# Kernel optimization log

Measured on AMD Instinct MI355X. Metric: run time of the kernel, lower is better.

The kernel has to match this reference:

```python
import jax, jax.numpy as jnp
import numpy as np

A, NL, LD, F, W, DEPTH = 128, 16, 256, 256, 1024, 4
CH, CHD = 8, 64   # cross-attn heads / head_dim
SH, SHD = 8, 32   # latent self-attn heads / head_dim
FF = 256          # 2**ceil(log2(latent_dim))
FLAT = NL * LD


def _ln(x, g, b, eps=1e-5):
    m = x.mean(-1, keepdims=True)
    v = ((x - m) ** 2).mean(-1, keepdims=True)
    return (x - m) * jax.lax.rsqrt(v + eps) * g + b


def _attn(q_in, kv, wq, wk, wv, wo, bo, h, hd):
    b, s, _ = q_in.shape
    t = kv.shape[1]
    q = (q_in @ wq.T).reshape(b, s, h, hd)
    k = (kv @ wk.T).reshape(b, t, h, hd)
    v = (kv @ wv.T).reshape(b, t, h, hd)
    p = jax.nn.softmax(jnp.einsum('bihd,bjhd->bhij', q, k) * (hd ** -0.5), axis=-1)
    o = jnp.einsum('bhij,bjhd->bihd', p, v).reshape(b, s, h * hd)
    return o @ wo.T + bo


def _block(q, kv, p, h, hd):
    wq, wk, wv, wo, bo, g1, b1, fw1, fb1, fw2, fb2, g2, b2 = p
    z = _ln(q + _attn(q, kv, wq, wk, wv, wo, bo, h, hd), g1, b1)
    ff = jax.nn.relu(z @ fw1.T + fb1) @ fw2.T + fb2
    return _ln(z + ff, g2, b2)


def setup_inputs() -> dict:
    key = jax.random.key(0)
    ks = iter(jax.random.split(key, 40))
    def rn(shape, s=0.02):
        return jax.random.normal(next(ks), shape, jnp.float32) * s
    return {
        'x': jax.random.normal(next(ks), (A, W, F), jnp.float32),
        'z': jax.random.normal(next(ks), (A, NL, LD), jnp.float32),
        'c_wq': rn((CH * CHD, LD)), 'c_wk': rn((CH * CHD, F)), 'c_wv': rn((CH * CHD, F)),
        'c_wo': rn((LD, CH * CHD)), 'c_bo': jnp.zeros((LD,), jnp.float32),
        'c_ln1_g': jnp.ones((LD,), jnp.float32), 'c_ln1_b': jnp.zeros((LD,), jnp.float32),
        'c_ff_w1': rn((FF, LD)), 'c_ff_b1': jnp.zeros((FF,), jnp.float32),
        'c_ff_w2': rn((LD, FF)), 'c_ff_b2': jnp.zeros((LD,), jnp.float32),
        'c_ln2_g': jnp.ones((LD,), jnp.float32), 'c_ln2_b': jnp.zeros((LD,), jnp.float32),
        's_wq': rn((DEPTH, SH * SHD, LD)), 's_wk': rn((DEPTH, SH * SHD, LD)),
        's_wv': rn((DEPTH, SH * SHD, LD)), 's_wo': rn((DEPTH, LD, SH * SHD)),
        's_bo': jnp.zeros((DEPTH, LD), jnp.float32),
        's_ln1_g': jnp.ones((DEPTH, LD), jnp.float32), 's_ln1_b': jnp.zeros((DEPTH, LD), jnp.float32),
        's_ff_w1': rn((DEPTH, FF, LD)), 's_ff_b1': jnp.zeros((DEPTH, FF), jnp.float32),
        's_ff_w2': rn((DEPTH, LD, FF)), 's_ff_b2': jnp.zeros((DEPTH, LD), jnp.float32),
        's_ln2_g': jnp.ones((DEPTH, LD), jnp.float32), 's_ln2_b': jnp.zeros((DEPTH, LD), jnp.float32),
        'q_w': rn((FLAT, FLAT)), 'q_b': jnp.zeros((FLAT,), jnp.float32),
        'k_w': rn((FLAT, FLAT)), 'k_b': jnp.zeros((FLAT,), jnp.float32),
        'v_w': rn((FLAT, FLAT)), 'v_b': jnp.zeros((FLAT,), jnp.float32),
    }


def reference(x, z, c_wq, c_wk, c_wv, c_wo, c_bo, c_ln1_g, c_ln1_b, c_ff_w1, c_ff_b1,
              c_ff_w2, c_ff_b2, c_ln2_g, c_ln2_b,
              s_wq, s_wk, s_wv, s_wo, s_bo, s_ln1_g, s_ln1_b, s_ff_w1, s_ff_b1,
              s_ff_w2, s_ff_b2, s_ln2_g, s_ln2_b,
              q_w, q_b, k_w, k_b, v_w, v_b):
    z_prior = z
    # NOTE: original LSRE.forward computes cross-attention but assigns the
    # result to x and never uses it. Replicated faithfully (dead computation;
    # output does not depend on x or the cross-attn params).
    _ = _block(z, x, (c_wq, c_wk, c_wv, c_wo, c_bo, c_ln1_g, c_ln1_b,
                      c_ff_w1, c_ff_b1, c_ff_w2, c_ff_b2, c_ln2_g, c_ln2_b), CH, CHD)
    zc = z
    sp = (s_wq, s_wk, s_wv, s_wo, s_bo, s_ln1_g, s_ln1_b,
          s_ff_w1, s_ff_b1, s_ff_w2, s_ff_b2, s_ln2_g, s_ln2_b)
    for i in range(DEPTH):
        zc = _block(zc, zc, tuple(p[i] for p in sp), SH, SHD)
    # CANN: asset-to-asset attention; broadcast-mul-then-sum == attn @ v
    zf = zc.reshape(A, FLAT)
    q = zf @ q_w.T + q_b
    k = zf @ k_w.T + k_b
    v = zf @ v_w.T + v_b
    attn = jax.nn.softmax((q @ k.T) * (LD ** -0.5), axis=-1)
    h = (attn @ v).reshape(A, NL, LD)
    return (h, z_prior)
```

## Files before the change

kernel.cpp:

```cpp
#include <hip/hip_runtime.h>
#include <math.h>

typedef __bf16 bf16x8 __attribute__((ext_vector_type(8)));
typedef __bf16 bf16x4 __attribute__((ext_vector_type(4)));
typedef float  f32x4  __attribute__((ext_vector_type(4)));

#define MFMA(a,b,c) __builtin_amdgcn_mfma_f32_16x16x32_bf16((a),(b),(c),0,0,0)

#define A_N   128
#define LDIM  256
#define FLATD 4096

__global__ void k_cvt_w(const float* __restrict__ s0, const float* __restrict__ s1,
                        const float* __restrict__ s2, const float* __restrict__ s3,
                        const float* __restrict__ s4, const float* __restrict__ s5,
                        __bf16* __restrict__ dh, __bf16* __restrict__ dl) {
    const float* s;
    switch (blockIdx.y) {
        case 0: s = s0; break; case 1: s = s1; break; case 2: s = s2; break;
        case 3: s = s3; break; case 4: s = s4; break; default: s = s5; break;
    }
    size_t off  = (size_t)blockIdx.x * 2048 + threadIdx.x * 8;
    const float4* sp = (const float4*)(s + off);
    float4 x = sp[0], y = sp[1];
    float v[8] = {x.x, x.y, x.z, x.w, y.x, y.y, y.z, y.w};
    bf16x8 h, l;
    #pragma unroll
    for (int j = 0; j < 8; ++j) {
        __bf16 hh = (__bf16)v[j];
        h[j] = hh;
        l[j] = (__bf16)(v[j] - (float)hh);
    }
    size_t dst = (size_t)blockIdx.y * 262144 + off;
    *(bf16x8*)(dh + dst) = h;
    *(bf16x8*)(dl + dst) = l;
}

__global__ __launch_bounds__(1024) void k_latent(
    const float* __restrict__ z,
    const __bf16* __restrict__ Wh, const __bf16* __restrict__ Wl,
    const float* __restrict__ boa,
    const float* __restrict__ g1a, const float* __restrict__ b1a,
    const float* __restrict__ fb1a, const float* __restrict__ fb2a,
    const float* __restrict__ g2a, const float* __restrict__ b2a,
    float* __restrict__ zprior, __bf16* __restrict__ Zbh, __bf16* __restrict__ Zbl)
{
    __shared__ __align__(16) char arena[57856];
    float*  zf  = (float*)arena;
    __bf16* zbh = (__bf16*)(arena + 16384);
    __bf16* zbl = (__bf16*)(arena + 24832);
    __bf16* Ph  = (__bf16*)(arena + 16384);
    __bf16* Qh  = (__bf16*)(arena + 33280);
    __bf16* ob  = Qh;
    __bf16* Kh  = (__bf16*)(arena + 41472);
    __bf16* Vt  = (__bf16*)(arena + 49664);

    const int a    = blockIdx.x;
    const int t    = threadIdx.x;
    const int w    = t >> 6;
    const int lane = t & 63;
    const int q    = lane >> 4;
    const int r    = lane & 15;
    const int nc   = w * 16;
    const int head = w >> 1;
    const int hc   = (w & 1) * 16;

    {
        int row = t >> 6, col = (t & 63) * 4;
        const float4 x = *(const float4*)(z + (size_t)a * 4096 + row * 256 + col);
        *(float4*)(zprior + (size_t)a * 4096 + row * 256 + col) = x;
        float v[4] = {x.x, x.y, x.z, x.w};
        float*  zr = zf  + row * 256 + col;
        __bf16* zh = zbh + row * 264 + col;
        __bf16* zl = zbl + row * 264 + col;
        #pragma unroll
        for (int j = 0; j < 4; ++j) {
            zr[j] = v[j];
            __bf16 hh = (__bf16)v[j];
            zh[j] = hh;
            zl[j] = (__bf16)(v[j] - (float)hh);
        }
    }
    __syncthreads();

    auto do_ln = [&](const float* g, const float* bb) {
        int col = lane * 4;
        float* zr = zf + w * 256 + col;
        float4 v4 = *(const float4*)zr;
        float v[4] = {v4.x, v4.y, v4.z, v4.w};
        float s1 = 0.f, s2 = 0.f;
        #pragma unroll
        for (int j = 0; j < 4; ++j) { s1 += v[j]; s2 += v[j]*v[j]; }
        #pragma unroll
        for (int o = 1; o <= 32; o <<= 1) {
            s1 += __shfl_xor(s1, o);
            s2 += __shfl_xor(s2, o);
        }
        float mean = s1 * (1.0f/256.0f);
        float var  = s2 * (1.0f/256.0f) - mean * mean;
        float inv  = rsqrtf(var + 1e-5f);
        float4 g4 = *(const float4*)(g + col);
        float4 b4 = *(const float4*)(bb + col);
        float gg[4] = {g4.x, g4.y, g4.z, g4.w};
        float bbv[4] = {b4.x, b4.y, b4.z, b4.w};
        __bf16* zh = zbh + w * 264 + col;
        __bf16* zl = zbl + w * 264 + col;
        float y[4];
        #pragma unroll
        for (int j = 0; j < 4; ++j) {
            y[j] = (v[j] - mean) * inv * gg[j] + bbv[j];
            __bf16 hh = (__bf16)y[j];
            zh[j] = hh;
            zl[j] = (__bf16)(y[j] - (float)hh);
        }
        *(float4*)zr = (float4){y[0], y[1], y[2], y[3]};
    };

    const f32x4 zero4 = {0.f, 0.f, 0.f, 0.f};
    bf16x8 zer8;
    #pragma unroll
    for (int j = 0; j < 8; ++j) zer8[j] = (__bf16)0.0f;

    for (int lp = 0; lp < 4; ++lp) {
        const size_t lo0 = (size_t)lp * 65536;
        const __bf16* wqh = Wh + 0*262144 + lo0; const __bf16* wql = Wl + 0*262144 + lo0;
        const __bf16* wkh = Wh + 1*262144 + lo0; const __bf16* wkl = Wl + 1*262144 + lo0;
        const __bf16* wvh = Wh + 2*262144 + lo0; const __bf16* wvl = Wl + 2*262144 + lo0;
        const __bf16* woh = Wh + 3*262144 + lo0; const __bf16* wol = Wl + 3*262144 + lo0;
        const __bf16* f1h = Wh + 4*262144 + lo0; const __bf16* f1l = Wl + 4*262144 + lo0;
        const __bf16* f2h = Wh + 5*262144 + lo0; const __bf16* f2l = Wl + 5*262144 + lo0;
        const float* bo  = boa  + lp*256;
        const float* g1  = g1a  + lp*256; const float* b1 = b1a + lp*256;
        const float* fb1 = fb1a + lp*256; const float* fb2 = fb2a + lp*256;
        const float* g2  = g2a  + lp*256; const float* b2 = b2a + lp*256;

        const size_t wrow = (size_t)(nc + r) * 256 + q * 8;
        const __bf16* zA_h = zbh + r * 264 + q * 8;
        const __bf16* zA_l = zbl + r * 264 + q * 8;
        const __bf16* oA   = ob  + r * 264 + q * 8;

        {
            const __bf16* pq_h = wqh + wrow; const __bf16* pq_l = wql + wrow;
            const __bf16* pk_h = wkh + wrow; const __bf16* pk_l = wkl + wrow;
            const __bf16* pv_h = wvh + wrow; const __bf16* pv_l = wvl + wrow;
            f32x4 aq = zero4, ak = zero4, av = zero4;
            #pragma unroll
            for (int ks = 0; ks < 8; ++ks) {
                bf16x8 afh = *(const bf16x8*)(zA_h + ks*32);
                bf16x8 afl = *(const bf16x8*)(zA_l + ks*32);
                bf16x8 qh = *(const bf16x8*)(pq_h + ks*32);
                bf16x8 ql = *(const bf16x8*)(pq_l + ks*32);
                bf16x8 kh = *(const bf16x8*)(pk_h + ks*32);
                bf16x8 kl = *(const bf16x8*)(pk_l + ks*32);
                bf16x8 vh = *(const bf16x8*)(pv_h + ks*32);
                bf16x8 vl = *(const bf16x8*)(pv_l + ks*32);
                aq = MFMA(afh, qh, aq); aq = MFMA(afl, qh, aq); aq = MFMA(afh, ql, aq);
                ak = MFMA(afh, kh, ak); ak = MFMA(afl, kh, ak); ak = MFMA(afh, kl, ak);
                av = MFMA(afh, vh, av); av = MFMA(afl, vh, av); av = MFMA(afh, vl, av);
            }
            #pragma unroll
            for (int i = 0; i < 4; ++i) {
                int m = q*4 + i;
                Qh[(head*16 + m)*32 + hc + r] = (__bf16)aq[i];
                Kh[(head*16 + m)*32 + hc + r] = (__bf16)ak[i];
                Vt[(head*32 + hc + r)*16 + m] = (__bf16)av[i];
            }
        }
        __syncthreads();

        if (w < 8) {
            bf16x8 qa = *(const bf16x8*)(Qh + (w*16 + r)*32 + q*8);
            bf16x8 ka = *(const bf16x8*)(Kh + (w*16 + r)*32 + q*8);
            f32x4 s = MFMA(qa, ka, zero4);
            #pragma unroll
            for (int i = 0; i < 4; ++i) {
                float sc = s[i] * 0.17677669529663687f;
                float mx = sc;
                #pragma unroll
                for (int o = 1; o <= 8; o <<= 1) mx = fmaxf(mx, __shfl_xor(mx, o, 16));
                float e = __expf(sc - mx);
                float sm = e;
                #pragma unroll
                for (int o = 1; o <= 8; o <<= 1) sm += __shfl_xor(sm, o, 16);
                Ph[(w*16 + q*4 + i)*32 + r]      = (__bf16)(e / sm);
                Ph[(w*16 + q*4 + i)*32 + 16 + r] = (__bf16)0.0f;
            }
        }
        __syncthreads();

        {
            int ph = w & 7, vnt = w >> 3;
            bf16x8 pa = *(const bf16x8*)(Ph + (ph*16 + r)*32 + q*8);
            bf16x8 vb = (q < 2)
                ? *(const bf16x8*)(Vt + (ph*32 + vnt*16 + r)*16 + q*8) : zer8;
            f32x4 o = MFMA(pa, vb, zero4);
            #pragma unroll
            for (int i = 0; i < 4; ++i)
                ob[(q*4 + i)*264 + ph*32 + vnt*16 + r] = (__bf16)o[i];
        }
        __syncthreads();

        {
            const __bf16* po_h = woh + wrow; const __bf16* po_l = wol + wrow;
            f32x4 acc = zero4;
            #pragma unroll
            for (int ks = 0; ks < 8; ++ks) {
                bf16x8 af = *(const bf16x8*)(oA + ks*32);
                bf16x8 bh = *(const bf16x8*)(po_h + ks*32);
                bf16x8 bl = *(const bf16x8*)(po_l + ks*32);
                acc = MFMA(af, bh, acc);
                acc = MFMA(af, bl, acc);
            }
            #pragma unroll
            for (int i = 0; i < 4; ++i) {
                int row = q*4 + i, col = nc + r;
                zf[row*256 + col] = acc[i] + bo[col] + zf[row*256 + col];
            }
        }
        __syncthreads();
        do_ln(g1, b1);
        __syncthreads();

        {
            const __bf16* pf_h = f1h + wrow; const __bf16* pf_l = f1l + wrow;
            f32x4 acc = zero4;
            #pragma unroll
            for (int ks = 0; ks < 8; ++ks) {
                bf16x8 afh = *(const bf16x8*)(zA_h + ks*32);
                bf16x8 afl = *(const bf16x8*)(zA_l + ks*32);
                bf16x8 bh  = *(const bf16x8*)(pf_h + ks*32);
                bf16x8 bl  = *(const bf16x8*)(pf_l + ks*32);
                acc = MFMA(afh, bh, acc);
                acc = MFMA(afl, bh, acc);
                acc = MFMA(afh, bl, acc);
            }
            #pragma unroll
            for (int i = 0; i < 4; ++i) {
                int row = q*4 + i, col = nc + r;
                ob[row*264 + col] = (__bf16)fmaxf(acc[i] + fb1[col], 0.0f);
            }
        }
        __syncthreads();

        {
            const __bf16* pf_h = f2h + wrow; const __bf16* pf_l = f2l + wrow;
            f32x4 acc = zero4;
            #pragma unroll
            for (int ks = 0; ks < 8; ++ks) {
                bf16x8 af = *(const bf16x8*)(oA + ks*32);
                bf16x8 bh = *(const bf16x8*)(pf_h + ks*32);
                bf16x8 bl = *(const bf16x8*)(pf_l + ks*32);
                acc = MFMA(af, bh, acc);
                acc = MFMA(af, bl, acc);
            }
            #pragma unroll
            for (int i = 0; i < 4; ++i) {
                int row = q*4 + i, col = nc + r;
                zf[row*256 + col] = acc[i] + fb2[col] + zf[row*256 + col];
            }
        }
        __syncthreads();
        do_ln(g2, b2);
        __syncthreads();
    }

    {
        int row = t >> 6, col = (t & 63) * 4;
        *(bf16x4*)(Zbh + (size_t)a * 4096 + row * 256 + col) =
            *(const bf16x4*)(zbh + row * 264 + col);
        *(bf16x4*)(Zbl + (size_t)a * 4096 + row * 256 + col) =
            *(const bf16x4*)(zbl + row * 264 + col);
    }
}

__global__ __launch_bounds__(256) void k_cann_gemm(
    const __bf16* __restrict__ Zh, const __bf16* __restrict__ Zl,
    const float* __restrict__ W0, const float* __restrict__ W1, const float* __restrict__ W2,
    const float* __restrict__ b0, const float* __restrict__ b1, const float* __restrict__ b2,
    float* __restrict__ C0, float* __restrict__ C1, float* __restrict__ C2)
{
    const float* W; const float* bias; float* C;
    if (blockIdx.y == 0)      { W = W0; bias = b0; C = C0; }
    else if (blockIdx.y == 1) { W = W1; bias = b1; C = C1; }
    else                      { W = W2; bias = b2; C = C2; }

    __shared__ __bf16 Ash[128 * 72];
    __shared__ __bf16 Asl[128 * 72];
    __shared__ __bf16 Bsh[32 * 72];
    __shared__ __bf16 Bsl[32 * 72];

    const int t = threadIdx.x;
    const int w = t >> 6, lane = t & 63, q = lane >> 4, r = lane & 15;
    const int n0 = blockIdx.x * 32;
    const int m0 = w * 32;
    const int br = t >> 3, bc = t & 7;

    const f32x4 zero4 = {0.f, 0.f, 0.f, 0.f};
    f32x4 acc[2][2] = {{zero4, zero4}, {zero4, zero4}};

    for (int k0 = 0; k0 < FLATD; k0 += 64) {
        #pragma unroll
        for (int l = 0; l < 4; ++l) {
            int idx = t + l * 256;
            int rr = idx >> 3, cc = idx & 7;
            *(bf16x8*)(Ash + rr*72 + cc*8) =
                *(const bf16x8*)(Zh + (size_t)rr * FLATD + k0 + cc*8);
            *(bf16x8*)(Asl + rr*72 + cc*8) =
                *(const bf16x8*)(Zl + (size_t)rr * FLATD + k0 + cc*8);
        }
        {
            const float4* wp = (const float4*)(W + (size_t)(n0 + br) * FLATD + k0 + bc*8);
            float4 x = wp[0], y = wp[1];
            float v[8] = {x.x, x.y, x.z, x.w, y.x, y.y, y.z, y.w};
            bf16x8 h, l;
            #pragma unroll
            for (int j = 0; j < 8; ++j) {
                __bf16 hh = (__bf16)v[j];
                h[j] = hh;
                l[j] = (__bf16)(v[j] - (float)hh);
            }
            *(bf16x8*)(Bsh + br*72 + bc*8) = h;
            *(bf16x8*)(Bsl + br*72 + bc*8) = l;
        }
        __syncthreads();
        #pragma unroll
        for (int ks = 0; ks < 2; ++ks) {
            bf16x8 a0h = *(const bf16x8*)(Ash + (m0 + r)*72      + ks*32 + q*8);
            bf16x8 a1h = *(const bf16x8*)(Ash + (m0 + 16 + r)*72 + ks*32 + q*8);
            bf16x8 a0l = *(const bf16x8*)(Asl + (m0 + r)*72      + ks*32 + q*8);
            bf16x8 a1l = *(const bf16x8*)(Asl + (m0 + 16 + r)*72 + ks*32 + q*8);
            bf16x8 g0h = *(const bf16x8*)(Bsh + r*72             + ks*32 + q*8);
            bf16x8 g1h = *(const bf16x8*)(Bsh + (16 + r)*72      + ks*32 + q*8);
            bf16x8 g0l = *(const bf16x8*)(Bsl + r*72             + ks*32 + q*8);
            bf16x8 g1l = *(const bf16x8*)(Bsl + (16 + r)*72      + ks*32 + q*8);
            acc[0][0] = MFMA(a0h, g0h, acc[0][0]);
            acc[0][0] = MFMA(a0l, g0h, acc[0][0]);
            acc[0][0] = MFMA(a0h, g0l, acc[0][0]);
            acc[0][1] = MFMA(a0h, g1h, acc[0][1]);
            acc[0][1] = MFMA(a0l, g1h, acc[0][1]);
            acc[0][1] = MFMA(a0h, g1l, acc[0][1]);
            acc[1][0] = MFMA(a1h, g0h, acc[1][0]);
            acc[1][0] = MFMA(a1l, g0h, acc[1][0]);
            acc[1][0] = MFMA(a1h, g0l, acc[1][0]);
            acc[1][1] = MFMA(a1h, g1h, acc[1][1]);
            acc[1][1] = MFMA(a1l, g1h, acc[1][1]);
            acc[1][1] = MFMA(a1h, g1l, acc[1][1]);
        }
        __syncthreads();
    }

    if (blockIdx.y == 1) {
        #pragma unroll
        for (int mi = 0; mi < 2; ++mi)
            #pragma unroll
            for (int ni = 0; ni < 2; ++ni)
                #pragma unroll
                for (int i = 0; i < 4; ++i) {
                    int row = m0 + mi*16 + q*4 + i;
                    int col = n0 + ni*16 + r;
                    C[(size_t)col * 128 + row] = acc[mi][ni][i] + bias[col];
                }
    } else {
        #pragma unroll
        for (int mi = 0; mi < 2; ++mi)
            #pragma unroll
            for (int ni = 0; ni < 2; ++ni)
                #pragma unroll
                for (int i = 0; i < 4; ++i) {
                    int row = m0 + mi*16 + q*4 + i;
                    int col = n0 + ni*16 + r;
                    C[(size_t)row * FLATD + col] = acc[mi][ni][i] + bias[col];
                }
    }
}

__global__ __launch_bounds__(512) void k_cann_scores(const float* __restrict__ Q,
                              const float* __restrict__ KT,
                              float* __restrict__ P) {
    const int i = blockIdx.x;
    const int t = threadIdx.x;
    __shared__ float qrow[FLATD];
    __shared__ float part[4][128];
    __shared__ float wred[2];
    __shared__ float wsum[2];
    {
        const float4* src = (const float4*)(Q + (size_t)i * FLATD);
        float4* dst = (float4*)qrow;
        dst[t]       = src[t];
        dst[t + 512] = src[t + 512];
    }
    __syncthreads();

    const int j = t & 127, quarter = t >> 7;
    const float* kp = KT + (size_t)quarter * 1024 * 128 + j;
    const float* qp = qrow + quarter * 1024;
    float sc = 0.0f;
    #pragma unroll 8
    for (int k = 0; k < 1024; ++k) sc += qp[k] * kp[(size_t)k * 128];
    part[quarter][j] = sc;
    __syncthreads();

    float v = 0.0f;
    if (t < 128) v = (part[0][j] + part[1][j] + part[2][j] + part[3][j]) * 0.0625f;

    float mx = (t < 128) ? v : -3.4e38f;
    #pragma unroll
    for (int o = 32; o; o >>= 1) mx = fmaxf(mx, __shfl_xor(mx, o));
    if (t < 128 && (t & 63) == 0) wred[t >> 6] = mx;
    __syncthreads();
    mx = fmaxf(wred[0], wred[1]);

    float e = (t < 128) ? __expf(v - mx) : 0.0f;
    float sum = e;
    #pragma unroll
    for (int o = 32; o; o >>= 1) sum += __shfl_xor(sum, o);
    if (t < 128 && (t & 63) == 0) wsum[t >> 6] = sum;
    __syncthreads();
    sum = wsum[0] + wsum[1];

    if (t < 128) P[(size_t)i * 128 + t] = e / sum;
}

__global__ void k_cann_out(const float* __restrict__ P,
                           const float* __restrict__ V,
                           float* __restrict__ H) {
    const int i = blockIdx.y;
    const int n = blockIdx.x * 256 + threadIdx.x;
    __shared__ float prow[128];
    if (threadIdx.x < 128) prow[threadIdx.x] = P[(size_t)i * 128 + threadIdx.x];
    __syncthreads();
    float acc = 0.0f;
    #pragma unroll 8
    for (int j = 0; j < 128; ++j) acc += prow[j] * V[(size_t)j * FLATD + n];
    H[(size_t)i * FLATD + n] = acc;
}

extern "C" void kernel_launch(void* const* d_in, const int* in_sizes, int n_in,
                              void* d_out, int out_size, void* d_ws, size_t ws_size,
                              hipStream_t stream) {
    (void)in_sizes; (void)n_in; (void)out_size; (void)ws_size;

    const float* z      = (const float*)d_in[1];
    const float* s_wq   = (const float*)d_in[15];
    const float* s_wk   = (const float*)d_in[16];
    const float* s_wv   = (const float*)d_in[17];
    const float* s_wo   = (const float*)d_in[18];
    const float* s_bo   = (const float*)d_in[19];
    const float* s_ln1g = (const float*)d_in[20];
    const float* s_ln1b = (const float*)d_in[21];
    const float* s_fw1  = (const float*)d_in[22];
    const float* s_fb1  = (const float*)d_in[23];
    const float* s_fw2  = (const float*)d_in[24];
    const float* s_fb2  = (const float*)d_in[25];
    const float* s_ln2g = (const float*)d_in[26];
    const float* s_ln2b = (const float*)d_in[27];
    const float* q_w    = (const float*)d_in[28];
    const float* q_b    = (const float*)d_in[29];
    const float* k_w    = (const float*)d_in[30];
    const float* k_b    = (const float*)d_in[31];
    const float* v_w    = (const float*)d_in[32];
    const float* v_b    = (const float*)d_in[33];

    float* out    = (float*)d_out;
    float* Hout   = out;
    float* Zprior = out + 524288;

    char* w8 = (char*)d_ws;
    __bf16* Wh  = (__bf16*)w8;
    __bf16* Wl  = (__bf16*)(w8 + 3145728);
    float*  Qb  = (float*)w8;
    float*  Kb  = (float*)(w8 + 2097152);
    float*  Vb  = (float*)(w8 + 4194304);
    __bf16* Zbh = (__bf16*)(w8 + 6291456);
    __bf16* Zbl = (__bf16*)(w8 + 7340032);
    float*  Pm  = (float*)(w8 + 8388608);

    k_cvt_w<<<dim3(128, 6), 256, 0, stream>>>(s_wq, s_wk, s_wv, s_wo, s_fw1, s_fw2,
                                              Wh, Wl);

    k_latent<<<A_N, 1024, 0, stream>>>(z, Wh, Wl, s_bo, s_ln1g, s_ln1b,
                                       s_fb1, s_fb2, s_ln2g, s_ln2b,
                                       Zprior, Zbh, Zbl);

    k_cann_gemm<<<dim3(FLATD / 32, 3), 256, 0, stream>>>(Zbh, Zbl, q_w, k_w, v_w,
                                                         q_b, k_b, v_b, Qb, Kb, Vb);

    k_cann_scores<<<A_N, 512, 0, stream>>>(Qb, Kb, Pm);
    k_cann_out<<<dim3(FLATD / 256, A_N), 256, 0, stream>>>(Pm, Vb, Hout);
}
```

Before: 623.7 us.

## Swizzle latent weights per-wave and register-block CANN score and output kernels

The weight conversion kernel now writes the hi/lo bf16 weights in a per-layer, per-wave interleaved layout. Each lane of k_latent can then read its MFMA B fragments as contiguous 512-element chunks instead of strided rows across six separate matrices, which improves coalescing and locality of the weight loads. The CANN scores kernel handles two query rows per block so each K load is reused twice. The output kernel computes an 8-row by 4-column register tile per thread so each V load is reused across 8 rows. The trade-off is fewer blocks, which lowers parallelism in the output kernel (64 blocks).

```diff
diff --git a/kernel.cpp b/kernel.cpp
--- a/kernel.cpp
+++ b/kernel.cpp
@@ -11,34 +11,46 @@
 #define LDIM  256
 #define FLATD 4096
 
-__global__ void k_cvt_w(const float* __restrict__ s0, const float* __restrict__ s1,
-                        const float* __restrict__ s2, const float* __restrict__ s3,
-                        const float* __restrict__ s4, const float* __restrict__ s5,
-                        __bf16* __restrict__ dh, __bf16* __restrict__ dl) {
+__global__ __launch_bounds__(256) void k_cvt_w(
+        const float* __restrict__ s0, const float* __restrict__ s1,
+        const float* __restrict__ s2, const float* __restrict__ s3,
+        const float* __restrict__ s4, const float* __restrict__ s5,
+        __bf16* __restrict__ W) {
+    const int g    = blockIdx.x * 256 + threadIdx.x;
+    const int lane = g & 63;
+    const int L    = g >> 6;
+    const int lp   = L / 1536;
+    const int rem  = L - lp * 1536;
+    const int w    = rem / 96;
+    const int li   = rem - w * 96;
+
+    int m, ks, hl;
+    if (li < 48)      { ks = li / 6; int sub = li - ks * 6; m = sub >> 1; hl = sub & 1; }
+    else if (li < 64) { int i = li - 48; m = 3; ks = i >> 1; hl = i & 1; }
+    else if (li < 80) { int i = li - 64; m = 4; ks = i >> 1; hl = i & 1; }
+    else              { int i = li - 80; m = 5; ks = i >> 1; hl = i & 1; }
+
     const float* s;
-    switch (blockIdx.y) {
+    switch (m) {
         case 0: s = s0; break; case 1: s = s1; break; case 2: s = s2; break;
         case 3: s = s3; break; case 4: s = s4; break; default: s = s5; break;
     }
-    size_t off  = (size_t)blockIdx.x * 2048 + threadIdx.x * 8;
-    const float4* sp = (const float4*)(s + off);
-    float4 x = sp[0], y = sp[1];
+    const float* src = s + lp * 65536 + (w * 16 + (lane & 15)) * 256
+                         + ks * 32 + (lane >> 4) * 8;
+    float4 x = ((const float4*)src)[0], y = ((const float4*)src)[1];
     float v[8] = {x.x, x.y, x.z, x.w, y.x, y.y, y.z, y.w};
-    bf16x8 h, l;
+    bf16x8 o;
     #pragma unroll
     for (int j = 0; j < 8; ++j) {
         __bf16 hh = (__bf16)v[j];
-        h[j] = hh;
-        l[j] = (__bf16)(v[j] - (float)hh);
-    }
-    size_t dst = (size_t)blockIdx.y * 262144 + off;
-    *(bf16x8*)(dh + dst) = h;
-    *(bf16x8*)(dl + dst) = l;
+        o[j] = hl ? (__bf16)(v[j] - (float)hh) : hh;
+    }
+    *(bf16x8*)(W + (size_t)g * 8) = o;
 }
 
 __global__ __launch_bounds__(1024) void k_latent(
     const float* __restrict__ z,
-    const __bf16* __restrict__ Wh, const __bf16* __restrict__ Wl,
+    const __bf16* __restrict__ Wswz,
     const float* __restrict__ boa,
     const float* __restrict__ g1a, const float* __restrict__ b1a,
     const float* __restrict__ fb1a, const float* __restrict__ fb2a,
@@ -122,38 +134,30 @@
     for (int j = 0; j < 8; ++j) zer8[j] = (__bf16)0.0f;
 
     for (int lp = 0; lp < 4; ++lp) {
-        const size_t lo0 = (size_t)lp * 65536;
-        const __bf16* wqh = Wh + 0*262144 + lo0; const __bf16* wql = Wl + 0*262144 + lo0;
-        const __bf16* wkh = Wh + 1*262144 + lo0; const __bf16* wkl = Wl + 1*262144 + lo0;
-        const __bf16* wvh = Wh + 2*262144 + lo0; const __bf16* wvl = Wl + 2*262144 + lo0;
-        const __bf16* woh = Wh + 3*262144 + lo0; const __bf16* wol = Wl + 3*262144 + lo0;
-        const __bf16* f1h = Wh + 4*262144 + lo0; const __bf16* f1l = Wl + 4*262144 + lo0;
-        const __bf16* f2h = Wh + 5*262144 + lo0; const __bf16* f2l = Wl + 5*262144 + lo0;
         const float* bo  = boa  + lp*256;
         const float* g1  = g1a  + lp*256; const float* b1 = b1a + lp*256;
         const float* fb1 = fb1a + lp*256; const float* fb2 = fb2a + lp*256;
         const float* g2  = g2a  + lp*256; const float* b2 = b2a + lp*256;
 
-        const size_t wrow = (size_t)(nc + r) * 256 + q * 8;
+        const __bf16* wsl = Wswz + (size_t)(lp * 16 + w) * 49152 + (size_t)lane * 8;
+        #define WCHUNK(idx) (*(const bf16x8*)(wsl + (idx) * 512))
+
         const __bf16* zA_h = zbh + r * 264 + q * 8;
         const __bf16* zA_l = zbl + r * 264 + q * 8;
         const __bf16* oA   = ob  + r * 264 + q * 8;
 
         {
-            const __bf16* pq_h = wqh + wrow; const __bf16* pq_l = wql + wrow;
-            const __bf16* pk_h = wkh + wrow; const __bf16* pk_l = wkl + wrow;
-            const __bf16* pv_h = wvh + wrow; const __bf16* pv_l = wvl + wrow;
             f32x4 aq = zero4, ak = zero4, av = zero4;
             #pragma unroll
             for (int ks = 0; ks < 8; ++ks) {
                 bf16x8 afh = *(const bf16x8*)(zA_h + ks*32);
                 bf16x8 afl = *(const bf16x8*)(zA_l + ks*32);
-                bf16x8 qh = *(const bf16x8*)(pq_h + ks*32);
-                bf16x8 ql = *(const bf16x8*)(pq_l + ks*32);
-                bf16x8 kh = *(const bf16x8*)(pk_h + ks*32);
-                bf16x8 kl = *(const bf16x8*)(pk_l + ks*32);
-                bf16x8 vh = *(const bf16x8*)(pv_h + ks*32);
-                bf16x8 vl = *(const bf16x8*)(pv_l + ks*32);
+                bf16x8 qh = WCHUNK(ks*6 + 0);
+                bf16x8 ql = WCHUNK(ks*6 + 1);
+                bf16x8 kh = WCHUNK(ks*6 + 2);
+                bf16x8 kl = WCHUNK(ks*6 + 3);
+                bf16x8 vh = WCHUNK(ks*6 + 4);
+                bf16x8 vl = WCHUNK(ks*6 + 5);
                 aq = MFMA(afh, qh, aq); aq = MFMA(afl, qh, aq); aq = MFMA(afh, ql, aq);
                 ak = MFMA(afh, kh, ak); ak = MFMA(afl, kh, ak); ak = MFMA(afh, kl, ak);
                 av = MFMA(afh, vh, av); av = MFMA(afl, vh, av); av = MFMA(afh, vl, av);
@@ -201,13 +205,12 @@
         __syncthreads();
 
         {
-            const __bf16* po_h = woh + wrow; const __bf16* po_l = wol + wrow;
             f32x4 acc = zero4;
             #pragma unroll
             for (int ks = 0; ks < 8; ++ks) {
                 bf16x8 af = *(const bf16x8*)(oA + ks*32);
-                bf16x8 bh = *(const bf16x8*)(po_h + ks*32);
-                bf16x8 bl = *(const bf16x8*)(po_l + ks*32);
+                bf16x8 bh = WCHUNK(48 + ks*2);
+                bf16x8 bl = WCHUNK(49 + ks*2);
                 acc = MFMA(af, bh, acc);
                 acc = MFMA(af, bl, acc);
             }
@@ -222,14 +225,13 @@
         __syncthreads();
 
         {
-            const __bf16* pf_h = f1h + wrow; const __bf16* pf_l = f1l + wrow;
             f32x4 acc = zero4;
             #pragma unroll
             for (int ks = 0; ks < 8; ++ks) {
                 bf16x8 afh = *(const bf16x8*)(zA_h + ks*32);
                 bf16x8 afl = *(const bf16x8*)(zA_l + ks*32);
-                bf16x8 bh  = *(const bf16x8*)(pf_h + ks*32);
-                bf16x8 bl  = *(const bf16x8*)(pf_l + ks*32);
+                bf16x8 bh  = WCHUNK(64 + ks*2);
+                bf16x8 bl  = WCHUNK(65 + ks*2);
                 acc = MFMA(afh, bh, acc);
                 acc = MFMA(afl, bh, acc);
                 acc = MFMA(afh, bl, acc);
@@ -243,13 +245,12 @@
         __syncthreads();
 
         {
-            const __bf16* pf_h = f2h + wrow; const __bf16* pf_l = f2l + wrow;
             f32x4 acc = zero4;
             #pragma unroll
             for (int ks = 0; ks < 8; ++ks) {
                 bf16x8 af = *(const bf16x8*)(oA + ks*32);
-                bf16x8 bh = *(const bf16x8*)(pf_h + ks*32);
-                bf16x8 bl = *(const bf16x8*)(pf_l + ks*32);
+                bf16x8 bh = WCHUNK(80 + ks*2);
+                bf16x8 bl = WCHUNK(81 + ks*2);
                 acc = MFMA(af, bh, acc);
                 acc = MFMA(af, bl, acc);
             }
@@ -262,6 +263,7 @@
         __syncthreads();
         do_ln(g2, b2);
         __syncthreads();
+        #undef WCHUNK
     }
 
     {
@@ -377,62 +379,95 @@
 __global__ __launch_bounds__(512) void k_cann_scores(const float* __restrict__ Q,
                               const float* __restrict__ KT,
                               float* __restrict__ P) {
-    const int i = blockIdx.x;
-    const int t = threadIdx.x;
-    __shared__ float qrow[FLATD];
-    __shared__ float part[4][128];
-    __shared__ float wred[2];
-    __shared__ float wsum[2];
+    const int i0 = blockIdx.x * 2;
+    const int t  = threadIdx.x;
+    __shared__ float qs[2][FLATD];
+    __shared__ float part[4][2][128];
+    __shared__ float wred[2][2];
+    __shared__ float wsum[2][2];
     {
-        const float4* src = (const float4*)(Q + (size_t)i * FLATD);
-        float4* dst = (float4*)qrow;
-        dst[t]       = src[t];
-        dst[t + 512] = src[t + 512];
+        const float4* src = (const float4*)(Q + (size_t)i0 * FLATD);
+        float4* dst = (float4*)qs;
+        #pragma unroll
+        for (int u = 0; u < 4; ++u) dst[t + u * 512] = src[t + u * 512];
     }
     __syncthreads();
 
-    const int j = t & 127, quarter = t >> 7;
-    const float* kp = KT + (size_t)quarter * 1024 * 128 + j;
-    const float* qp = qrow + quarter * 1024;
-    float sc = 0.0f;
+    const int j = t & 127, ksub = t >> 7;
+    const float* kp = KT + (size_t)(ksub * 1024) * 128 + j;
+    const float* q0 = qs[0] + ksub * 1024;
+    const float* q1 = qs[1] + ksub * 1024;
+    float a0 = 0.0f, a1 = 0.0f;
     #pragma unroll 8
-    for (int k = 0; k < 1024; ++k) sc += qp[k] * kp[(size_t)k * 128];
-    part[quarter][j] = sc;
+    for (int k = 0; k < 1024; ++k) {
+        float kv = kp[(size_t)k * 128];
+        a0 += q0[k] * kv;
+        a1 += q1[k] * kv;
+    }
+    part[ksub][0][j] = a0;
+    part[ksub][1][j] = a1;
     __syncthreads();
 
-    float v = 0.0f;
-    if (t < 128) v = (part[0][j] + part[1][j] + part[2][j] + part[3][j]) * 0.0625f;
-
-    float mx = (t < 128) ? v : -3.4e38f;
+    float v = 0.0f, e = 0.0f;
+    const int i = t >> 7;
+    if (t < 256)
+        v = (part[0][i][j] + part[1][i][j] + part[2][i][j] + part[3][i][j]) * 0.0625f;
+
+    float mx = (t < 256) ? v : -3.4e38f;
     #pragma unroll
     for (int o = 32; o; o >>= 1) mx = fmaxf(mx, __shfl_xor(mx, o));
-    if (t < 128 && (t & 63) == 0) wred[t >> 6] = mx;
+    if (t < 256 && (j & 63) == 0) wred[i][j >> 6] = mx;
     __syncthreads();
-    mx = fmaxf(wred[0], wred[1]);
-
-    float e = (t < 128) ? __expf(v - mx) : 0.0f;
+    if (t < 256) {
+        mx = fmaxf(wred[i][0], wred[i][1]);
+        e = __expf(v - mx);
+    }
     float sum = e;
     #pragma unroll
     for (int o = 32; o; o >>= 1) sum += __shfl_xor(sum, o);
-    if (t < 128 && (t & 63) == 0) wsum[t >> 6] = sum;
+    if (t < 256 && (j & 63) == 0) wsum[i][j >> 6] = sum;
     __syncthreads();
-    sum = wsum[0] + wsum[1];
-
-    if (t < 128) P[(size_t)i * 128 + t] = e / sum;
+    if (t < 256) {
+        sum = wsum[i][0] + wsum[i][1];
+        P[(size_t)(i0 + i) * 128 + j] = e / sum;
+    }
 }
 
-__global__ void k_cann_out(const float* __restrict__ P,
+__global__ __launch_bounds__(256) void k_cann_out(const float* __restrict__ P,
                            const float* __restrict__ V,
                            float* __restrict__ H) {
-    const int i = blockIdx.y;
-    const int n = blockIdx.x * 256 + threadIdx.x;
-    __shared__ float prow[128];
-    if (threadIdx.x < 128) prow[threadIdx.x] = P[(size_t)i * 128 + threadIdx.x];
+    const int i0 = blockIdx.y * 8;
+    const int t  = threadIdx.x;
+    const int nb = blockIdx.x * 1024 + t * 4;
+    __shared__ float ps[128][8];
+    #pragma unroll
+    for (int u = 0; u < 4; ++u) {
+        int e = t + u * 256;
+        int i = e >> 7, j = e & 127;
+        ps[j][i] = P[(size_t)(i0 + i) * 128 + j];
+    }
     __syncthreads();
-    float acc = 0.0f;
-    #pragma unroll 8
-    for (int j = 0; j < 128; ++j) acc += prow[j] * V[(size_t)j * FLATD + n];
-    H[(size_t)i * FLATD + n] = acc;
+
+    f32x4 acc[8];
+    #pragma unroll
+    for (int i = 0; i < 8; ++i) acc[i] = (f32x4){0.f, 0.f, 0.f, 0.f};
+
+    for (int j = 0; j < 128; ++j) {
+        float4 vv = *(const float4*)(V + (size_t)j * FLATD + nb);
+        f32x4 v4 = {vv.x, vv.y, vv.z, vv.w};
+        float4 pa = *(const float4*)&ps[j][0];
+        float4 pb = *(const float4*)&ps[j][4];
+        acc[0] += pa.x * v4; acc[1] += pa.y * v4;
+        acc[2] += pa.z * v4; acc[3] += pa.w * v4;
+        acc[4] += pb.x * v4; acc[5] += pb.y * v4;
+        acc[6] += pb.z * v4; acc[7] += pb.w * v4;
+    }
+    #pragma unroll
+    for (int i = 0; i < 8; ++i) {
+        f32x4 a = acc[i];
+        *(float4*)(H + (size_t)(i0 + i) * FLATD + nb) =
+            (float4){a[0], a[1], a[2], a[3]};
+    }
 }
 
 extern "C" void kernel_launch(void* const* d_in, const int* in_sizes, int n_in,
@@ -466,8 +501,7 @@
     float* Zprior = out + 524288;
 
     char* w8 = (char*)d_ws;
-    __bf16* Wh  = (__bf16*)w8;
-    __bf16* Wl  = (__bf16*)(w8 + 3145728);
+    __bf16* Wswz = (__bf16*)w8;
     float*  Qb  = (float*)w8;
     float*  Kb  = (float*)(w8 + 2097152);
     float*  Vb  = (float*)(w8 + 4194304);
@@ -475,16 +509,15 @@
     __bf16* Zbl = (__bf16*)(w8 + 7340032);
     float*  Pm  = (float*)(w8 + 8388608);
 
-    k_cvt_w<<<dim3(128, 6), 256, 0, stream>>>(s_wq, s_wk, s_wv, s_wo, s_fw1, s_fw2,
-                                              Wh, Wl);
-
-    k_latent<<<A_N, 1024, 0, stream>>>(z, Wh, Wl, s_bo, s_ln1g, s_ln1b,
+    k_cvt_w<<<1536, 256, 0, stream>>>(s_wq, s_wk, s_wv, s_wo, s_fw1, s_fw2, Wswz);
+
+    k_latent<<<A_N, 1024, 0, stream>>>(z, Wswz, s_bo, s_ln1g, s_ln1b,
                                        s_fb1, s_fb2, s_ln2g, s_ln2b,
                                        Zprior, Zbh, Zbl);
 
     k_cann_gemm<<<dim3(FLATD / 32, 3), 256, 0, stream>>>(Zbh, Zbl, q_w, k_w, v_w,
                                                          q_b, k_b, v_b, Qb, Kb, Vb);
 
-    k_cann_scores<<<A_N, 512, 0, stream>>>(Qb, Kb, Pm);
-    k_cann_out<<<dim3(FLATD / 256, A_N), 256, 0, stream>>>(Pm, Vb, Hout);
+    k_cann_scores<<<A_N / 2, 512, 0, stream>>>(Qb, Kb, Pm);
+    k_cann_out<<<dim3(4, 16), 256, 0, stream>>>(Pm, Vb, Hout);
 }
```

New measurement: 522.0 us. -16.3%, faster.
